# Optimization experiments

Measured on AMD Instinct MI355X. Metric: run time of the kernel, lower is better.

The kernel has to match this reference:

```python
import jax, jax.numpy as jnp
import numpy as np


def setup_inputs() -> dict:
    key = jax.random.key(0)
    k = jax.random.split(key, 5)
    B, S, D, H = 4, 2048, 2048, 8192
    scale1 = 1.0 / np.sqrt(D)
    scale2 = 1.0 / np.sqrt(H)
    return {
        "x": jax.random.normal(k[0], (B, S, D), dtype=jnp.float32),
        "w1": jax.random.normal(k[1], (H, D), dtype=jnp.float32) * scale1,
        "b1": jax.random.normal(k[2], (H,), dtype=jnp.float32) * scale1,
        "w2": jax.random.normal(k[3], (D, H), dtype=jnp.float32) * scale2,
        "b2": jax.random.normal(k[4], (D,), dtype=jnp.float32) * scale2,
    }


def reference(x, w1, b1, w2, b2):
    # fc1: [B,S,D] @ [D,H] -> [B,S,H]
    h = jnp.einsum("bsd,hd->bsh", x, w1) + b1
    # squared ReLU activation
    a = jnp.square(jax.nn.relu(h))
    # fc2: [B,S,H] @ [H,D] -> [B,S,D]
    return jnp.einsum("bsh,dh->bsd", a, w2) + b2
```

## Files before the change

### kernel.cpp

```cpp
#include <hip/hip_runtime.h>
#include <hip/hip_bf16.h>
#include <stdint.h>

typedef __bf16 bf16x8 __attribute__((ext_vector_type(8)));
typedef float f32x4 __attribute__((ext_vector_type(4)));


__device__ inline void gload_lds16(const void* g, void* lds) {
  __builtin_amdgcn_global_load_lds(
      (const __attribute__((address_space(1))) uint32_t*)(uintptr_t)g,
      (__attribute__((address_space(3))) uint32_t*)(uintptr_t)lds,
      16, 0, 0);
}

__device__ inline bf16x8 ds_readv(uint32_t addr) {
  bf16x8 r;
  asm volatile("ds_read_b128 %0, %1" : "=v"(r) : "v"(addr));
  return r;
}

#define LGKM(N) do {                                             \
    asm volatile("s_waitcnt lgkmcnt(" #N ")" ::: "memory");      \
    __builtin_amdgcn_sched_barrier(0);                           \
  } while (0)

__device__ inline short f2bf(float f) {
  union { float f; uint32_t u; } x; x.f = f;
  uint32_t u = x.u;
  u += 0x7fffu + ((u >> 16) & 1u);
  return (short)(u >> 16);
}

#define BAR() do { asm volatile("" ::: "memory"); \
                   __builtin_amdgcn_s_barrier();  \
                   asm volatile("" ::: "memory"); } while (0)


__global__ __launch_bounds__(256) void cvt_f32_bf16(
    const float* __restrict__ in, short* __restrict__ out, int n4) {
  int i = blockIdx.x * 256 + threadIdx.x;
  if (i < n4) {
    float4 v = reinterpret_cast<const float4*>(in)[i];
    short4 o;
    o.x = f2bf(v.x); o.y = f2bf(v.y); o.z = f2bf(v.z); o.w = f2bf(v.w);
    reinterpret_cast<short4*>(out)[i] = o;
  }
}


template <int EPI>
__global__ __launch_bounds__(512, 2) void gemm_bt(
    const short* __restrict__ A, const short* __restrict__ B,
    const float* __restrict__ bias, void* __restrict__ Cout,
    int M, int N, int K) {
  __shared__ __align__(16) short lds[2][4][128 * 64];

  const int tid  = threadIdx.x;
  const int wave = tid >> 6;
  const int lane = tid & 63;
  const int wr = wave >> 2;
  const int wc = wave & 3;
  const int fr = lane & 15, kq = lane >> 4;

  const int nwg = gridDim.x;
  const int w = (blockIdx.x & 7) * (nwg >> 3) + (blockIdx.x >> 3);
  const int gy = M >> 8;
  const int brow = w % gy;
  const int bcol = w / gy;

  f32x4 acc[8][4];
#pragma unroll
  for (int m = 0; m < 8; ++m)
#pragma unroll
    for (int n = 0; n < 4; ++n)
      acc[m][n] = (f32x4){0.f, 0.f, 0.f, 0.f};

  const int nk = K >> 6;

  const uint32_t LB = (uint32_t)(uintptr_t)&lds[0][0][0];
  uint32_t aA[4][2], aB[2][2];
#pragma unroll
  for (int m = 0; m < 4; ++m)
#pragma unroll
    for (int kk = 0; kk < 2; ++kk) {
      int r = wr * 64 + m * 16 + fr;
      int g = r * 8 + kk * 4 + kq;
      aA[m][kk] = LB + (uint32_t)((g ^ (r & 7)) * 16);
    }
#pragma unroll
  for (int n = 0; n < 2; ++n)
#pragma unroll
    for (int kk = 0; kk < 2; ++kk) {
      int r = wc * 32 + n * 16 + fr;
      int g = r * 8 + kk * 4 + kq;
      aB[n][kk] = LB + (uint32_t)((g ^ (r & 7)) * 16);
    }

  const int i0 = tid;
  const int gl0 = i0 ^ ((i0 >> 3) & 7);
  const int r0 = gl0 >> 3, c0 = gl0 & 7;
  const size_t rstep = (size_t)128 * K;

  const short* pA[2];
  const short* pB[2];
  {
    const int rb0 = (r0 >> 5) * 64 + (r0 & 31);
#pragma unroll
    for (int h = 0; h < 2; ++h) {
      pA[h] = A + (size_t)(brow * 256 + h * 64 + r0) * K + c0 * 8;
      pB[h] = B + (size_t)(bcol * 256 + rb0 + h * 32) * K + c0 * 8;
    }
  }

  const int dst0 = wave * 512, dst1 = 4096 + wave * 512;

#define STAGE(p, buf, slot)                              \
  do {                                                   \
    short* base_ = &lds[buf][slot][0];                   \
    gload_lds16((p), base_ + dst0);                      \
    gload_lds16((p) + rstep, base_ + dst1);              \
    (p) += 64;                                           \
  } while (0)

  STAGE(pA[0], 0, 0);
  STAGE(pA[1], 0, 1);
  STAGE(pB[0], 0, 2);
  STAGE(pB[1], 0, 3);
  asm volatile("s_waitcnt vmcnt(0)" ::: "memory");
  BAR();

  for (int t = 0; t < nk; ++t) {
    const int cur = t & 1, nxt = cur ^ 1;
    const bool s1 = (t + 1) < nk;

    if (s1) {
      STAGE(pA[0], nxt, 0);
      STAGE(pA[1], nxt, 1);
      STAGE(pB[0], nxt, 2);
      STAGE(pB[1], nxt, 3);
    }

    const uint32_t cb = (uint32_t)cur << 16;

    bf16x8 bq0[2][2], a0q[4][2], a1q[4][2], bq1[2][2];
#pragma unroll
    for (int n = 0; n < 2; ++n)
#pragma unroll
      for (int kk = 0; kk < 2; ++kk)
        bq0[n][kk] = ds_readv(aB[n][kk] + cb + 32768u);
#pragma unroll
    for (int m = 0; m < 4; ++m)
#pragma unroll
      for (int kk = 0; kk < 2; ++kk)
        a0q[m][kk] = ds_readv(aA[m][kk] + cb);
#pragma unroll
    for (int m = 0; m < 4; ++m)
#pragma unroll
      for (int kk = 0; kk < 2; ++kk)
        a1q[m][kk] = ds_readv(aA[m][kk] + cb + 16384u);
#pragma unroll
    for (int n = 0; n < 2; ++n)
#pragma unroll
      for (int kk = 0; kk < 2; ++kk)
        bq1[n][kk] = ds_readv(aB[n][kk] + cb + 49152u);

    LGKM(12);
    __builtin_amdgcn_s_setprio(1);
#pragma unroll
    for (int m = 0; m < 4; ++m)
#pragma unroll
      for (int n = 0; n < 2; ++n)
#pragma unroll
        for (int kk = 0; kk < 2; ++kk)
          acc[m][n] = __builtin_amdgcn_mfma_f32_16x16x32_bf16(
              bq0[n][kk], a0q[m][kk], acc[m][n], 0, 0, 0);
    __builtin_amdgcn_s_setprio(0);

    LGKM(4);
    __builtin_amdgcn_s_setprio(1);
#pragma unroll
    for (int m = 0; m < 4; ++m)
#pragma unroll
      for (int n = 0; n < 2; ++n)
#pragma unroll
        for (int kk = 0; kk < 2; ++kk)
          acc[m + 4][n] = __builtin_amdgcn_mfma_f32_16x16x32_bf16(
              bq0[n][kk], a1q[m][kk], acc[m + 4][n], 0, 0, 0);
    __builtin_amdgcn_s_setprio(0);

    LGKM(0);
    __builtin_amdgcn_s_setprio(1);
#pragma unroll
    for (int m = 0; m < 4; ++m)
#pragma unroll
      for (int n = 0; n < 2; ++n)
#pragma unroll
        for (int kk = 0; kk < 2; ++kk)
          acc[m + 4][n + 2] = __builtin_amdgcn_mfma_f32_16x16x32_bf16(
              bq1[n][kk], a1q[m][kk], acc[m + 4][n + 2], 0, 0, 0);
    __builtin_amdgcn_s_setprio(0);
    __builtin_amdgcn_s_setprio(1);
#pragma unroll
    for (int m = 0; m < 4; ++m)
#pragma unroll
      for (int n = 0; n < 2; ++n)
#pragma unroll
        for (int kk = 0; kk < 2; ++kk)
          acc[m][n + 2] = __builtin_amdgcn_mfma_f32_16x16x32_bf16(
              bq1[n][kk], a0q[m][kk], acc[m][n + 2], 0, 0, 0);
    __builtin_amdgcn_s_setprio(0);

    if (s1) {
      asm volatile("s_waitcnt vmcnt(0)" ::: "memory");
      BAR();
    }
  }

  const int q = lane >> 4;
  if (EPI == 0) {
    short* C = (short*)Cout;
#pragma unroll
    for (int m = 0; m < 8; ++m) {
      const int row = brow * 256 + wr * 128 + m * 16 + fr;
#pragma unroll
      for (int n = 0; n < 4; ++n) {
        const int col = bcol * 256 + wc * 64 + n * 16 + q * 4;
        const float4 bv = *(const float4*)&bias[col];
        short4 o;
        float v0 = acc[m][n][0] + bv.x; v0 = v0 > 0.f ? v0 * v0 : 0.f;
        float v1 = acc[m][n][1] + bv.y; v1 = v1 > 0.f ? v1 * v1 : 0.f;
        float v2 = acc[m][n][2] + bv.z; v2 = v2 > 0.f ? v2 * v2 : 0.f;
        float v3 = acc[m][n][3] + bv.w; v3 = v3 > 0.f ? v3 * v3 : 0.f;
        o.x = f2bf(v0); o.y = f2bf(v1); o.z = f2bf(v2); o.w = f2bf(v3);
        *(short4*)&C[(size_t)row * N + col] = o;
      }
    }
  } else {
    float* C = (float*)Cout;
#pragma unroll
    for (int m = 0; m < 8; ++m) {
      const int row = brow * 256 + wr * 128 + m * 16 + fr;
#pragma unroll
      for (int n = 0; n < 4; ++n) {
        const int col = bcol * 256 + wc * 64 + n * 16 + q * 4;
        const float4 bv = *(const float4*)&bias[col];
        float4 o;
        o.x = acc[m][n][0] + bv.x;
        o.y = acc[m][n][1] + bv.y;
        o.z = acc[m][n][2] + bv.z;
        o.w = acc[m][n][3] + bv.w;
        *(float4*)&C[(size_t)row * N + col] = o;
      }
    }
  }
#undef STAGE
}


extern "C" void kernel_launch(void* const* d_in, const int* in_sizes, int n_in,
                              void* d_out, int out_size, void* d_ws,
                              size_t ws_size, hipStream_t stream) {
  const float* x  = (const float*)d_in[0];
  const float* w1 = (const float*)d_in[1];
  const float* b1 = (const float*)d_in[2];
  const float* w2 = (const float*)d_in[3];
  const float* b2 = (const float*)d_in[4];
  float* out = (float*)d_out;

  const int H = in_sizes[2];
  const int D = in_sizes[4];
  const int M = in_sizes[0] / D;

  short* xb  = (short*)d_ws;
  short* w1b = xb  + (size_t)M * D;
  short* w2b = w1b + (size_t)H * D;
  short* act = w2b + (size_t)D * H;

  {
    int n4 = (M * D) / 4;
    cvt_f32_bf16<<<(n4 + 255) / 256, 256, 0, stream>>>(x, xb, n4);
    n4 = (H * D) / 4;
    cvt_f32_bf16<<<(n4 + 255) / 256, 256, 0, stream>>>(w1, w1b, n4);
    n4 = (D * H) / 4;
    cvt_f32_bf16<<<(n4 + 255) / 256, 256, 0, stream>>>(w2, w2b, n4);
  }

  gemm_bt<0><<<(M / 256) * (H / 256), 512, 0, stream>>>(
      xb, w1b, b1, (void*)act, M, H, D);
  gemm_bt<1><<<(M / 256) * (D / 256), 512, 0, stream>>>(
      act, w2b, b2, (void*)out, M, D, H);
}
```

Measured before the change: 572.7 us.

## Restructure GEMM main loop into 8-phase pipelined schedule with per-slot staging

Replaces the simple double-buffered K loop, which staged a whole tile and then waited on vmcnt(0) plus a barrier, with an unrolled two-tile schedule. Each tile is split into four MFMA quadrants, and each quadrant phase issues the global-to-LDS load for one sub-slot and waits with partial vmcnt counts. The aim is to overlap memory transfers with MFMA work at a finer grain and avoid full drains each iteration. In exchange there are many more barriers per tile, and correctness depends on the slot-reuse ordering and an even K tile count.

```diff
diff --git a/kernel.cpp b/kernel.cpp
--- a/kernel.cpp
+++ b/kernel.cpp
@@ -21,6 +21,10 @@
 
 #define LGKM(N) do {                                             \
     asm volatile("s_waitcnt lgkmcnt(" #N ")" ::: "memory");      \
+    __builtin_amdgcn_sched_barrier(0);                           \
+  } while (0)
+#define VM(N) do {                                               \
+    asm volatile("s_waitcnt vmcnt(" #N ")" ::: "memory");        \
     __builtin_amdgcn_sched_barrier(0);                           \
   } while (0)
 
@@ -122,50 +126,8 @@
     (p) += 64;                                           \
   } while (0)
 
-  STAGE(pA[0], 0, 0);
-  STAGE(pA[1], 0, 1);
-  STAGE(pB[0], 0, 2);
-  STAGE(pB[1], 0, 3);
-  asm volatile("s_waitcnt vmcnt(0)" ::: "memory");
-  BAR();
-
-  for (int t = 0; t < nk; ++t) {
-    const int cur = t & 1, nxt = cur ^ 1;
-    const bool s1 = (t + 1) < nk;
-
-    if (s1) {
-      STAGE(pA[0], nxt, 0);
-      STAGE(pA[1], nxt, 1);
-      STAGE(pB[0], nxt, 2);
-      STAGE(pB[1], nxt, 3);
-    }
-
-    const uint32_t cb = (uint32_t)cur << 16;
-
-    bf16x8 bq0[2][2], a0q[4][2], a1q[4][2], bq1[2][2];
-#pragma unroll
-    for (int n = 0; n < 2; ++n)
-#pragma unroll
-      for (int kk = 0; kk < 2; ++kk)
-        bq0[n][kk] = ds_readv(aB[n][kk] + cb + 32768u);
-#pragma unroll
-    for (int m = 0; m < 4; ++m)
-#pragma unroll
-      for (int kk = 0; kk < 2; ++kk)
-        a0q[m][kk] = ds_readv(aA[m][kk] + cb);
-#pragma unroll
-    for (int m = 0; m < 4; ++m)
-#pragma unroll
-      for (int kk = 0; kk < 2; ++kk)
-        a1q[m][kk] = ds_readv(aA[m][kk] + cb + 16384u);
-#pragma unroll
-    for (int n = 0; n < 2; ++n)
-#pragma unroll
-      for (int kk = 0; kk < 2; ++kk)
-        bq1[n][kk] = ds_readv(aB[n][kk] + cb + 49152u);
-
-    LGKM(12);
-    __builtin_amdgcn_s_setprio(1);
+  bf16x8 a0q[4][2], a1q[4][2], bq0[2][2], bq1[2][2];
+  auto Q1 = [&]() {
 #pragma unroll
     for (int m = 0; m < 4; ++m)
 #pragma unroll
@@ -174,10 +136,28 @@
         for (int kk = 0; kk < 2; ++kk)
           acc[m][n] = __builtin_amdgcn_mfma_f32_16x16x32_bf16(
               bq0[n][kk], a0q[m][kk], acc[m][n], 0, 0, 0);
-    __builtin_amdgcn_s_setprio(0);
-
-    LGKM(4);
-    __builtin_amdgcn_s_setprio(1);
+  };
+  auto Q2 = [&]() {
+#pragma unroll
+    for (int m = 0; m < 4; ++m)
+#pragma unroll
+      for (int n = 0; n < 2; ++n)
+#pragma unroll
+        for (int kk = 0; kk < 2; ++kk)
+          acc[m][n + 2] = __builtin_amdgcn_mfma_f32_16x16x32_bf16(
+              bq1[n][kk], a0q[m][kk], acc[m][n + 2], 0, 0, 0);
+  };
+  auto Q3 = [&]() {
+#pragma unroll
+    for (int m = 0; m < 4; ++m)
+#pragma unroll
+      for (int n = 0; n < 2; ++n)
+#pragma unroll
+        for (int kk = 0; kk < 2; ++kk)
+          acc[m + 4][n + 2] = __builtin_amdgcn_mfma_f32_16x16x32_bf16(
+              bq1[n][kk], a1q[m][kk], acc[m + 4][n + 2], 0, 0, 0);
+  };
+  auto Q4 = [&]() {
 #pragma unroll
     for (int m = 0; m < 4; ++m)
 #pragma unroll
@@ -186,35 +166,120 @@
         for (int kk = 0; kk < 2; ++kk)
           acc[m + 4][n] = __builtin_amdgcn_mfma_f32_16x16x32_bf16(
               bq0[n][kk], a1q[m][kk], acc[m + 4][n], 0, 0, 0);
-    __builtin_amdgcn_s_setprio(0);
-
-    LGKM(0);
-    __builtin_amdgcn_s_setprio(1);
-#pragma unroll
-    for (int m = 0; m < 4; ++m)
-#pragma unroll
-      for (int n = 0; n < 2; ++n)
-#pragma unroll
-        for (int kk = 0; kk < 2; ++kk)
-          acc[m + 4][n + 2] = __builtin_amdgcn_mfma_f32_16x16x32_bf16(
-              bq1[n][kk], a1q[m][kk], acc[m + 4][n + 2], 0, 0, 0);
-    __builtin_amdgcn_s_setprio(0);
-    __builtin_amdgcn_s_setprio(1);
-#pragma unroll
-    for (int m = 0; m < 4; ++m)
-#pragma unroll
-      for (int n = 0; n < 2; ++n)
-#pragma unroll
-        for (int kk = 0; kk < 2; ++kk)
-          acc[m][n + 2] = __builtin_amdgcn_mfma_f32_16x16x32_bf16(
-              bq1[n][kk], a0q[m][kk], acc[m][n + 2], 0, 0, 0);
-    __builtin_amdgcn_s_setprio(0);
-
-    if (s1) {
-      asm volatile("s_waitcnt vmcnt(0)" ::: "memory");
-      BAR();
-    }
-  }
+  };
+  auto RD_A0 = [&](uint32_t cb) {
+#pragma unroll
+    for (int m = 0; m < 4; ++m)
+#pragma unroll
+      for (int kk = 0; kk < 2; ++kk)
+        a0q[m][kk] = ds_readv(aA[m][kk] + cb);
+  };
+  auto RD_A1 = [&](uint32_t cb) {
+#pragma unroll
+    for (int m = 0; m < 4; ++m)
+#pragma unroll
+      for (int kk = 0; kk < 2; ++kk)
+        a1q[m][kk] = ds_readv(aA[m][kk] + cb + 16384u);
+  };
+  auto RD_B0 = [&](uint32_t cb) {
+#pragma unroll
+    for (int n = 0; n < 2; ++n)
+#pragma unroll
+      for (int kk = 0; kk < 2; ++kk)
+        bq0[n][kk] = ds_readv(aB[n][kk] + cb + 32768u);
+  };
+  auto RD_B1 = [&](uint32_t cb) {
+#pragma unroll
+    for (int n = 0; n < 2; ++n)
+#pragma unroll
+      for (int kk = 0; kk < 2; ++kk)
+        bq1[n][kk] = ds_readv(aB[n][kk] + cb + 49152u);
+  };
+
+#define PRIO_ON  __builtin_amdgcn_s_setprio(1)
+#define PRIO_OFF __builtin_amdgcn_s_setprio(0)
+
+  STAGE(pA[0], 0, 0);
+  STAGE(pB[0], 0, 2);
+  STAGE(pB[1], 0, 3);
+  STAGE(pA[1], 0, 1);
+  STAGE(pA[0], 1, 0);
+  STAGE(pB[0], 1, 2);
+  STAGE(pB[1], 1, 3);
+  VM(6);
+  BAR();
+
+  const int niter = nk >> 1;
+  for (int i = 0; i < niter - 1; ++i) {
+    RD_A0(0); RD_B0(0);
+    STAGE(pA[1], 1, 1);
+    LGKM(8);
+    BAR();
+    LGKM(0);
+    PRIO_ON; Q1(); PRIO_OFF;
+    VM(10); BAR();
+    RD_B1(0);
+    STAGE(pA[0], 0, 0);
+    BAR();
+    LGKM(0);
+    PRIO_ON; Q2(); PRIO_OFF;
+    VM(10); BAR();
+    RD_A1(0);
+    STAGE(pB[0], 0, 2);
+    BAR();
+    LGKM(0);
+    PRIO_ON; Q3(); PRIO_OFF;
+    VM(10); BAR();
+    STAGE(pB[1], 0, 3);
+    BAR();
+    PRIO_ON; Q4(); PRIO_OFF;
+    VM(10); BAR();
+
+    RD_A0(65536u); RD_B0(65536u);
+    STAGE(pA[1], 0, 1);
+    LGKM(8);
+    BAR();
+    LGKM(0);
+    PRIO_ON; Q1(); PRIO_OFF;
+    VM(10); BAR();
+    RD_B1(65536u);
+    STAGE(pA[0], 1, 0);
+    BAR();
+    LGKM(0);
+    PRIO_ON; Q2(); PRIO_OFF;
+    VM(10); BAR();
+    RD_A1(65536u);
+    STAGE(pB[0], 1, 2);
+    BAR();
+    LGKM(0);
+    PRIO_ON; Q3(); PRIO_OFF;
+    VM(10); BAR();
+    STAGE(pB[1], 1, 3);
+    BAR();
+    PRIO_ON; Q4(); PRIO_OFF;
+    VM(10); BAR();
+  }
+
+  RD_A0(0); RD_B0(0);
+  STAGE(pA[1], 1, 1);
+  LGKM(8);
+  BAR();
+  LGKM(0);
+  PRIO_ON; Q1(); PRIO_OFF;
+  VM(0); BAR();
+  RD_B1(0); BAR(); LGKM(0);
+  PRIO_ON; Q2(); PRIO_OFF; BAR();
+  RD_A1(0); BAR(); LGKM(0);
+  PRIO_ON; Q3(); PRIO_OFF; BAR();
+  PRIO_ON; Q4(); PRIO_OFF;
+  BAR();
+  RD_A0(65536u); RD_B0(65536u); BAR(); LGKM(0);
+  PRIO_ON; Q1(); PRIO_OFF; BAR();
+  RD_B1(65536u); BAR(); LGKM(0);
+  PRIO_ON; Q2(); PRIO_OFF; BAR();
+  RD_A1(65536u); BAR(); LGKM(0);
+  PRIO_ON; Q3(); PRIO_OFF; BAR();
+  PRIO_ON; Q4(); PRIO_OFF;
 
   const int q = lane >> 4;
   if (EPI == 0) {
```

Result: faster. 544.4 us (median of 3 runs) (-4.9%).

## Switch GEMM to 32x32x16 MFMA with quadrant-interleaved staged prefetch pipeline

Applied to the files above, without the earlier changes.

Replaces the 16x16x32 MFMA tiles with 32x32x16 tiles, so each wave holds 4x2 accumulator fragments of 16 floats and reads LDS with immediate offsets from precomputed swizzled bases. The main loop is split into four compute quadrants. Global-to-LDS loads for the next k-tiles are issued piecemeal between them, and the buffer slots are refilled as soon as each is consumed, with partial vmcnt waits instead of a full drain. This aims to overlap memory with MFMA work and cut LDS read traffic, at the cost of more barriers per iteration and more delicate slot-reuse correctness.

```diff
diff --git a/kernel.cpp b/kernel.cpp
--- a/kernel.cpp
+++ b/kernel.cpp
@@ -3,7 +3,7 @@
 #include <stdint.h>
 
 typedef __bf16 bf16x8 __attribute__((ext_vector_type(8)));
-typedef float f32x4 __attribute__((ext_vector_type(4)));
+typedef float f32x16 __attribute__((ext_vector_type(16)));
 
 
 __device__ inline void gload_lds16(const void* g, void* lds) {
@@ -13,14 +13,20 @@
       16, 0, 0);
 }
 
-__device__ inline bf16x8 ds_readv(uint32_t addr) {
-  bf16x8 r;
-  asm volatile("ds_read_b128 %0, %1" : "=v"(r) : "v"(addr));
-  return r;
-}
+#define DSR(dst, base, OFF)                                         \
+  asm volatile("ds_read_b128 %0, %1 offset:" #OFF                   \
+               : "=v"(dst) : "v"(base))
+#define RD4(arr, base, OFF) do {                                    \
+    DSR(arr[0], base[0], OFF); DSR(arr[1], base[1], OFF);           \
+    DSR(arr[2], base[2], OFF); DSR(arr[3], base[3], OFF);           \
+  } while (0)
 
 #define LGKM(N) do {                                             \
     asm volatile("s_waitcnt lgkmcnt(" #N ")" ::: "memory");      \
+    __builtin_amdgcn_sched_barrier(0);                           \
+  } while (0)
+#define VM(N) do {                                               \
+    asm volatile("s_waitcnt vmcnt(" #N ")" ::: "memory");        \
     __builtin_amdgcn_sched_barrier(0);                           \
   } while (0)
 
@@ -60,7 +66,7 @@
   const int lane = tid & 63;
   const int wr = wave >> 2;
   const int wc = wave & 3;
-  const int fr = lane & 15, kq = lane >> 4;
+  const int l31 = lane & 31, kh = lane >> 5;
 
   const int nwg = gridDim.x;
   const int w = (blockIdx.x & 7) * (nwg >> 3) + (blockIdx.x >> 3);
@@ -68,33 +74,31 @@
   const int brow = w % gy;
   const int bcol = w / gy;
 
-  f32x4 acc[8][4];
-#pragma unroll
-  for (int m = 0; m < 8; ++m)
-#pragma unroll
-    for (int n = 0; n < 4; ++n)
-      acc[m][n] = (f32x4){0.f, 0.f, 0.f, 0.f};
+  f32x16 acc[4][2];
+#pragma unroll
+  for (int m = 0; m < 4; ++m)
+#pragma unroll
+    for (int n = 0; n < 2; ++n) {
+      f32x16 z = {0.f};
+      acc[m][n] = z;
+    }
 
   const int nk = K >> 6;
 
   const uint32_t LB = (uint32_t)(uintptr_t)&lds[0][0][0];
-  uint32_t aA[4][2], aB[2][2];
-#pragma unroll
-  for (int m = 0; m < 4; ++m)
-#pragma unroll
-    for (int kk = 0; kk < 2; ++kk) {
-      int r = wr * 64 + m * 16 + fr;
-      int g = r * 8 + kk * 4 + kq;
-      aA[m][kk] = LB + (uint32_t)((g ^ (r & 7)) * 16);
-    }
-#pragma unroll
-  for (int n = 0; n < 2; ++n)
-#pragma unroll
-    for (int kk = 0; kk < 2; ++kk) {
-      int r = wc * 32 + n * 16 + fr;
-      int g = r * 8 + kk * 4 + kq;
-      aB[n][kk] = LB + (uint32_t)((g ^ (r & 7)) * 16);
-    }
+  uint32_t aT[4], bT[4];
+  {
+    const int r  = wr * 64 + l31;
+    const int x  = r & 7;
+    const int rb = wc * 32 + l31;
+    const int xb = rb & 7;
+#pragma unroll
+    for (int ks = 0; ks < 4; ++ks) {
+      aT[ks] = LB + (uint32_t)(r * 128 + (((ks * 2 + kh) ^ x) * 16));
+      bT[ks] = LB + 32768u +
+               (uint32_t)(rb * 128 + (((ks * 2 + kh) ^ xb) * 16));
+    }
+  }
 
   const int i0 = tid;
   const int gl0 = i0 ^ ((i0 >> 3) & 7);
@@ -122,134 +126,137 @@
     (p) += 64;                                           \
   } while (0)
 
+  bf16x8 a01[2][4], a23[2][4], b0[4], b1[4];
+  auto Q1 = [&]() {
+#pragma unroll
+    for (int mi = 0; mi < 2; ++mi)
+#pragma unroll
+      for (int ks = 0; ks < 4; ++ks)
+        acc[mi][0] = __builtin_amdgcn_mfma_f32_32x32x16_bf16(
+            b0[ks], a01[mi][ks], acc[mi][0], 0, 0, 0);
+  };
+  auto Q2 = [&]() {
+#pragma unroll
+    for (int mi = 0; mi < 2; ++mi)
+#pragma unroll
+      for (int ks = 0; ks < 4; ++ks)
+        acc[mi][1] = __builtin_amdgcn_mfma_f32_32x32x16_bf16(
+            b1[ks], a01[mi][ks], acc[mi][1], 0, 0, 0);
+  };
+  auto Q3 = [&]() {
+#pragma unroll
+    for (int mi = 0; mi < 2; ++mi)
+#pragma unroll
+      for (int ks = 0; ks < 4; ++ks)
+        acc[2 + mi][1] = __builtin_amdgcn_mfma_f32_32x32x16_bf16(
+            b1[ks], a23[mi][ks], acc[2 + mi][1], 0, 0, 0);
+  };
+  auto Q4 = [&]() {
+#pragma unroll
+    for (int mi = 0; mi < 2; ++mi)
+#pragma unroll
+      for (int ks = 0; ks < 4; ++ks)
+        acc[2 + mi][0] = __builtin_amdgcn_mfma_f32_32x32x16_bf16(
+            b0[ks], a23[mi][ks], acc[2 + mi][0], 0, 0, 0);
+  };
+
+#define PRIO_ON  __builtin_amdgcn_s_setprio(1)
+#define PRIO_OFF __builtin_amdgcn_s_setprio(0)
+
   STAGE(pA[0], 0, 0);
-  STAGE(pA[1], 0, 1);
   STAGE(pB[0], 0, 2);
   STAGE(pB[1], 0, 3);
-  asm volatile("s_waitcnt vmcnt(0)" ::: "memory");
+  STAGE(pA[1], 0, 1);
+  STAGE(pA[0], 1, 0);
+  STAGE(pB[0], 1, 2);
+  STAGE(pB[1], 1, 3);
+  VM(6);
   BAR();
 
   for (int t = 0; t < nk; ++t) {
     const int cur = t & 1, nxt = cur ^ 1;
-    const bool s1 = (t + 1) < nk;
-
-    if (s1) {
-      STAGE(pA[0], nxt, 0);
-      STAGE(pA[1], nxt, 1);
-      STAGE(pB[0], nxt, 2);
-      STAGE(pB[1], nxt, 3);
-    }
-
-    const uint32_t cb = (uint32_t)cur << 16;
-
-    bf16x8 bq0[2][2], a0q[4][2], a1q[4][2], bq1[2][2];
-#pragma unroll
-    for (int n = 0; n < 2; ++n)
-#pragma unroll
-      for (int kk = 0; kk < 2; ++kk)
-        bq0[n][kk] = ds_readv(aB[n][kk] + cb + 32768u);
-#pragma unroll
-    for (int m = 0; m < 4; ++m)
-#pragma unroll
-      for (int kk = 0; kk < 2; ++kk)
-        a0q[m][kk] = ds_readv(aA[m][kk] + cb);
-#pragma unroll
-    for (int m = 0; m < 4; ++m)
-#pragma unroll
-      for (int kk = 0; kk < 2; ++kk)
-        a1q[m][kk] = ds_readv(aA[m][kk] + cb + 16384u);
-#pragma unroll
-    for (int n = 0; n < 2; ++n)
-#pragma unroll
-      for (int kk = 0; kk < 2; ++kk)
-        bq1[n][kk] = ds_readv(aB[n][kk] + cb + 49152u);
-
-    LGKM(12);
-    __builtin_amdgcn_s_setprio(1);
-#pragma unroll
-    for (int m = 0; m < 4; ++m)
-#pragma unroll
-      for (int n = 0; n < 2; ++n)
-#pragma unroll
-        for (int kk = 0; kk < 2; ++kk)
-          acc[m][n] = __builtin_amdgcn_mfma_f32_16x16x32_bf16(
-              bq0[n][kk], a0q[m][kk], acc[m][n], 0, 0, 0);
-    __builtin_amdgcn_s_setprio(0);
-
-    LGKM(4);
-    __builtin_amdgcn_s_setprio(1);
-#pragma unroll
-    for (int m = 0; m < 4; ++m)
-#pragma unroll
-      for (int n = 0; n < 2; ++n)
-#pragma unroll
-        for (int kk = 0; kk < 2; ++kk)
-          acc[m + 4][n] = __builtin_amdgcn_mfma_f32_16x16x32_bf16(
-              bq0[n][kk], a1q[m][kk], acc[m + 4][n], 0, 0, 0);
-    __builtin_amdgcn_s_setprio(0);
-
+    const bool s1 = (t + 1) < nk, g2 = (t + 2) < nk;
+    if (t) {
+      const int32_t d = cur ? 65536 : -65536;
+#pragma unroll
+      for (int ks = 0; ks < 4; ++ks) { aT[ks] += d; bT[ks] += d; }
+    }
+
+    RD4(a01[0], aT, 0);
+    RD4(a01[1], aT, 4096);
+    RD4(b0, bT, 0);
+    if (s1) STAGE(pA[1], nxt, 1);
+    LGKM(8);
+    BAR();
     LGKM(0);
-    __builtin_amdgcn_s_setprio(1);
-#pragma unroll
-    for (int m = 0; m < 4; ++m)
-#pragma unroll
-      for (int n = 0; n < 2; ++n)
-#pragma unroll
-        for (int kk = 0; kk < 2; ++kk)
-          acc[m + 4][n + 2] = __builtin_amdgcn_mfma_f32_16x16x32_bf16(
-              bq1[n][kk], a1q[m][kk], acc[m + 4][n + 2], 0, 0, 0);
-    __builtin_amdgcn_s_setprio(0);
-    __builtin_amdgcn_s_setprio(1);
-#pragma unroll
-    for (int m = 0; m < 4; ++m)
-#pragma unroll
-      for (int n = 0; n < 2; ++n)
-#pragma unroll
-        for (int kk = 0; kk < 2; ++kk)
-          acc[m][n + 2] = __builtin_amdgcn_mfma_f32_16x16x32_bf16(
-              bq1[n][kk], a0q[m][kk], acc[m][n + 2], 0, 0, 0);
-    __builtin_amdgcn_s_setprio(0);
-
-    if (s1) {
-      asm volatile("s_waitcnt vmcnt(0)" ::: "memory");
-      BAR();
-    }
-  }
-
-  const int q = lane >> 4;
+    PRIO_ON; Q1(); PRIO_OFF;
+    BAR();
+
+    RD4(b1, bT, 16384);
+    if (g2) STAGE(pA[0], cur, 0);
+    BAR();
+    LGKM(0);
+    PRIO_ON; Q2(); PRIO_OFF;
+    BAR();
+
+    RD4(a23[0], aT, 16384);
+    RD4(a23[1], aT, 20480);
+    if (g2) STAGE(pB[0], cur, 2);
+    BAR();
+    LGKM(0);
+    PRIO_ON; Q3(); PRIO_OFF;
+    BAR();
+
+    if (g2) STAGE(pB[1], cur, 3);
+    BAR();
+    PRIO_ON; Q4(); PRIO_OFF;
+    if (g2)      { VM(6); }
+    else if (s1) { VM(0); }
+    if (s1) BAR();
+  }
+
+  const int hi = lane >> 5;
   if (EPI == 0) {
     short* C = (short*)Cout;
 #pragma unroll
-    for (int m = 0; m < 8; ++m) {
-      const int row = brow * 256 + wr * 128 + m * 16 + fr;
-#pragma unroll
-      for (int n = 0; n < 4; ++n) {
-        const int col = bcol * 256 + wc * 64 + n * 16 + q * 4;
-        const float4 bv = *(const float4*)&bias[col];
-        short4 o;
-        float v0 = acc[m][n][0] + bv.x; v0 = v0 > 0.f ? v0 * v0 : 0.f;
-        float v1 = acc[m][n][1] + bv.y; v1 = v1 > 0.f ? v1 * v1 : 0.f;
-        float v2 = acc[m][n][2] + bv.z; v2 = v2 > 0.f ? v2 * v2 : 0.f;
-        float v3 = acc[m][n][3] + bv.w; v3 = v3 > 0.f ? v3 * v3 : 0.f;
-        o.x = f2bf(v0); o.y = f2bf(v1); o.z = f2bf(v2); o.w = f2bf(v3);
-        *(short4*)&C[(size_t)row * N + col] = o;
+    for (int mf = 0; mf < 4; ++mf) {
+      const int row = brow * 256 + wr * 128 + mf * 32 + l31;
+#pragma unroll
+      for (int nf = 0; nf < 2; ++nf) {
+        const int colb = bcol * 256 + wc * 64 + nf * 32 + hi * 4;
+#pragma unroll
+        for (int g = 0; g < 4; ++g) {
+          const int col = colb + g * 8;
+          const float4 bv = *(const float4*)&bias[col];
+          short4 o;
+          float v0 = acc[mf][nf][4 * g + 0] + bv.x; v0 = v0 > 0.f ? v0 * v0 : 0.f;
+          float v1 = acc[mf][nf][4 * g + 1] + bv.y; v1 = v1 > 0.f ? v1 * v1 : 0.f;
+          float v2 = acc[mf][nf][4 * g + 2] + bv.z; v2 = v2 > 0.f ? v2 * v2 : 0.f;
+          float v3 = acc[mf][nf][4 * g + 3] + bv.w; v3 = v3 > 0.f ? v3 * v3 : 0.f;
+          o.x = f2bf(v0); o.y = f2bf(v1); o.z = f2bf(v2); o.w = f2bf(v3);
+          *(short4*)&C[(size_t)row * N + col] = o;
+        }
       }
     }
   } else {
     float* C = (float*)Cout;
 #pragma unroll
-    for (int m = 0; m < 8; ++m) {
-      const int row = brow * 256 + wr * 128 + m * 16 + fr;
-#pragma unroll
-      for (int n = 0; n < 4; ++n) {
-        const int col = bcol * 256 + wc * 64 + n * 16 + q * 4;
-        const float4 bv = *(const float4*)&bias[col];
-        float4 o;
-        o.x = acc[m][n][0] + bv.x;
-        o.y = acc[m][n][1] + bv.y;
-        o.z = acc[m][n][2] + bv.z;
-        o.w = acc[m][n][3] + bv.w;
-        *(float4*)&C[(size_t)row * N + col] = o;
+    for (int mf = 0; mf < 4; ++mf) {
+      const int row = brow * 256 + wr * 128 + mf * 32 + l31;
+#pragma unroll
+      for (int nf = 0; nf < 2; ++nf) {
+        const int colb = bcol * 256 + wc * 64 + nf * 32 + hi * 4;
+#pragma unroll
+        for (int g = 0; g < 4; ++g) {
+          const int col = colb + g * 8;
+          const float4 bv = *(const float4*)&bias[col];
+          float4 o;
+          o.x = acc[mf][nf][4 * g + 0] + bv.x;
+          o.y = acc[mf][nf][4 * g + 1] + bv.y;
+          o.z = acc[mf][nf][4 * g + 2] + bv.z;
+          o.w = acc[mf][nf][4 * g + 3] + bv.w;
+          *(float4*)&C[(size_t)row * N + col] = o;
+        }
       }
     }
   }
```

Result: slower. 650.5 us (+13.6%).

## Interleave per-quadrant LDS reads, global prefetch and MFMA with finer barriers

Applied to the files above, without the earlier changes.

The main loop is reorganised into four compute quadrants. Each quadrant loads its own LDS fragments and issues one slot of the next tile's global-to-LDS prefetch, so slots are refilled as soon as they are consumed. The prologue now prefetches most of two k-tiles ahead, and vmcnt waits are partial rather than full drains. LDS addresses use base registers plus immediate offsets instead of per-fragment address arrays, which cuts VGPR use. The cost is many more workgroup barriers per iteration and tricky slot-reuse ordering, which could cause stalls or races if any dependency is mis-sequenced.

```diff
diff --git a/kernel.cpp b/kernel.cpp
--- a/kernel.cpp
+++ b/kernel.cpp
@@ -13,14 +13,16 @@
       16, 0, 0);
 }
 
-__device__ inline bf16x8 ds_readv(uint32_t addr) {
-  bf16x8 r;
-  asm volatile("ds_read_b128 %0, %1" : "=v"(r) : "v"(addr));
-  return r;
-}
+#define DSR(dst, base, OFF)                                         \
+  asm volatile("ds_read_b128 %0, %1 offset:" #OFF                   \
+               : "=v"(dst) : "v"(base))
 
 #define LGKM(N) do {                                             \
     asm volatile("s_waitcnt lgkmcnt(" #N ")" ::: "memory");      \
+    __builtin_amdgcn_sched_barrier(0);                           \
+  } while (0)
+#define VM(N) do {                                               \
+    asm volatile("s_waitcnt vmcnt(" #N ")" ::: "memory");        \
     __builtin_amdgcn_sched_barrier(0);                           \
   } while (0)
 
@@ -78,23 +80,15 @@
   const int nk = K >> 6;
 
   const uint32_t LB = (uint32_t)(uintptr_t)&lds[0][0][0];
-  uint32_t aA[4][2], aB[2][2];
-#pragma unroll
-  for (int m = 0; m < 4; ++m)
-#pragma unroll
-    for (int kk = 0; kk < 2; ++kk) {
-      int r = wr * 64 + m * 16 + fr;
-      int g = r * 8 + kk * 4 + kq;
-      aA[m][kk] = LB + (uint32_t)((g ^ (r & 7)) * 16);
-    }
-#pragma unroll
-  for (int n = 0; n < 2; ++n)
-#pragma unroll
-    for (int kk = 0; kk < 2; ++kk) {
-      int r = wc * 32 + n * 16 + fr;
-      int g = r * 8 + kk * 4 + kq;
-      aB[n][kk] = LB + (uint32_t)((g ^ (r & 7)) * 16);
-    }
+  uint32_t bA[2], bB[2];
+  {
+    const uint32_t x0 = (uint32_t)(((kq)     ^ (fr & 7)) * 16);
+    const uint32_t x1 = (uint32_t)(((4 + kq) ^ (fr & 7)) * 16);
+    const uint32_t ra = (uint32_t)((wr * 64 + fr) * 128);
+    const uint32_t rb = (uint32_t)((wc * 32 + fr) * 128);
+    bA[0] = LB + ra + x0;            bA[1] = LB + ra + x1;
+    bB[0] = LB + 32768u + rb + x0;   bB[1] = LB + 32768u + rb + x1;
+  }
 
   const int i0 = tid;
   const int gl0 = i0 ^ ((i0 >> 3) & 7);
@@ -122,98 +116,106 @@
     (p) += 64;                                           \
   } while (0)
 
+  bf16x8 a0q[4][2], a1q[4][2], bq0[2][2], bq1[2][2];
+  auto Q1 = [&]() {
+#pragma unroll
+    for (int m = 0; m < 4; ++m)
+#pragma unroll
+      for (int n = 0; n < 2; ++n)
+#pragma unroll
+        for (int kk = 0; kk < 2; ++kk)
+          acc[m][n] = __builtin_amdgcn_mfma_f32_16x16x32_bf16(
+              bq0[n][kk], a0q[m][kk], acc[m][n], 0, 0, 0);
+  };
+  auto Q2 = [&]() {
+#pragma unroll
+    for (int m = 0; m < 4; ++m)
+#pragma unroll
+      for (int n = 0; n < 2; ++n)
+#pragma unroll
+        for (int kk = 0; kk < 2; ++kk)
+          acc[m][n + 2] = __builtin_amdgcn_mfma_f32_16x16x32_bf16(
+              bq1[n][kk], a0q[m][kk], acc[m][n + 2], 0, 0, 0);
+  };
+  auto Q3 = [&]() {
+#pragma unroll
+    for (int m = 0; m < 4; ++m)
+#pragma unroll
+      for (int n = 0; n < 2; ++n)
+#pragma unroll
+        for (int kk = 0; kk < 2; ++kk)
+          acc[m + 4][n + 2] = __builtin_amdgcn_mfma_f32_16x16x32_bf16(
+              bq1[n][kk], a1q[m][kk], acc[m + 4][n + 2], 0, 0, 0);
+  };
+  auto Q4 = [&]() {
+#pragma unroll
+    for (int m = 0; m < 4; ++m)
+#pragma unroll
+      for (int n = 0; n < 2; ++n)
+#pragma unroll
+        for (int kk = 0; kk < 2; ++kk)
+          acc[m + 4][n] = __builtin_amdgcn_mfma_f32_16x16x32_bf16(
+              bq0[n][kk], a1q[m][kk], acc[m + 4][n], 0, 0, 0);
+  };
+
+#define PRIO_ON  __builtin_amdgcn_s_setprio(1)
+#define PRIO_OFF __builtin_amdgcn_s_setprio(0)
+
   STAGE(pA[0], 0, 0);
-  STAGE(pA[1], 0, 1);
   STAGE(pB[0], 0, 2);
   STAGE(pB[1], 0, 3);
-  asm volatile("s_waitcnt vmcnt(0)" ::: "memory");
+  STAGE(pA[1], 0, 1);
+  STAGE(pA[0], 1, 0);
+  STAGE(pB[0], 1, 2);
+  STAGE(pB[1], 1, 3);
+  VM(6);
   BAR();
 
   for (int t = 0; t < nk; ++t) {
     const int cur = t & 1, nxt = cur ^ 1;
-    const bool s1 = (t + 1) < nk;
-
-    if (s1) {
-      STAGE(pA[0], nxt, 0);
-      STAGE(pA[1], nxt, 1);
-      STAGE(pB[0], nxt, 2);
-      STAGE(pB[1], nxt, 3);
-    }
-
-    const uint32_t cb = (uint32_t)cur << 16;
-
-    bf16x8 bq0[2][2], a0q[4][2], a1q[4][2], bq1[2][2];
-#pragma unroll
-    for (int n = 0; n < 2; ++n)
-#pragma unroll
-      for (int kk = 0; kk < 2; ++kk)
-        bq0[n][kk] = ds_readv(aB[n][kk] + cb + 32768u);
-#pragma unroll
-    for (int m = 0; m < 4; ++m)
-#pragma unroll
-      for (int kk = 0; kk < 2; ++kk)
-        a0q[m][kk] = ds_readv(aA[m][kk] + cb);
-#pragma unroll
-    for (int m = 0; m < 4; ++m)
-#pragma unroll
-      for (int kk = 0; kk < 2; ++kk)
-        a1q[m][kk] = ds_readv(aA[m][kk] + cb + 16384u);
-#pragma unroll
-    for (int n = 0; n < 2; ++n)
-#pragma unroll
-      for (int kk = 0; kk < 2; ++kk)
-        bq1[n][kk] = ds_readv(aB[n][kk] + cb + 49152u);
-
-    LGKM(12);
-    __builtin_amdgcn_s_setprio(1);
-#pragma unroll
-    for (int m = 0; m < 4; ++m)
-#pragma unroll
-      for (int n = 0; n < 2; ++n)
-#pragma unroll
-        for (int kk = 0; kk < 2; ++kk)
-          acc[m][n] = __builtin_amdgcn_mfma_f32_16x16x32_bf16(
-              bq0[n][kk], a0q[m][kk], acc[m][n], 0, 0, 0);
-    __builtin_amdgcn_s_setprio(0);
-
-    LGKM(4);
-    __builtin_amdgcn_s_setprio(1);
-#pragma unroll
-    for (int m = 0; m < 4; ++m)
-#pragma unroll
-      for (int n = 0; n < 2; ++n)
-#pragma unroll
-        for (int kk = 0; kk < 2; ++kk)
-          acc[m + 4][n] = __builtin_amdgcn_mfma_f32_16x16x32_bf16(
-              bq0[n][kk], a1q[m][kk], acc[m + 4][n], 0, 0, 0);
-    __builtin_amdgcn_s_setprio(0);
-
+    const bool s1 = (t + 1) < nk, g2 = (t + 2) < nk;
+    if (t) {
+      const int32_t d = cur ? 65536 : -65536;
+      bA[0] += d; bA[1] += d; bB[0] += d; bB[1] += d;
+    }
+
+    DSR(a0q[0][0], bA[0], 0);     DSR(a0q[0][1], bA[1], 0);
+    DSR(a0q[1][0], bA[0], 2048);  DSR(a0q[1][1], bA[1], 2048);
+    DSR(a0q[2][0], bA[0], 4096);  DSR(a0q[2][1], bA[1], 4096);
+    DSR(a0q[3][0], bA[0], 6144);  DSR(a0q[3][1], bA[1], 6144);
+    DSR(bq0[0][0], bB[0], 0);     DSR(bq0[0][1], bB[1], 0);
+    DSR(bq0[1][0], bB[0], 2048);  DSR(bq0[1][1], bB[1], 2048);
+    if (s1) STAGE(pA[1], nxt, 1);
+    LGKM(8);
+    BAR();
     LGKM(0);
-    __builtin_amdgcn_s_setprio(1);
-#pragma unroll
-    for (int m = 0; m < 4; ++m)
-#pragma unroll
-      for (int n = 0; n < 2; ++n)
-#pragma unroll
-        for (int kk = 0; kk < 2; ++kk)
-          acc[m + 4][n + 2] = __builtin_amdgcn_mfma_f32_16x16x32_bf16(
-              bq1[n][kk], a1q[m][kk], acc[m + 4][n + 2], 0, 0, 0);
-    __builtin_amdgcn_s_setprio(0);
-    __builtin_amdgcn_s_setprio(1);
-#pragma unroll
-    for (int m = 0; m < 4; ++m)
-#pragma unroll
-      for (int n = 0; n < 2; ++n)
-#pragma unroll
-        for (int kk = 0; kk < 2; ++kk)
-          acc[m][n + 2] = __builtin_amdgcn_mfma_f32_16x16x32_bf16(
-              bq1[n][kk], a0q[m][kk], acc[m][n + 2], 0, 0, 0);
-    __builtin_amdgcn_s_setprio(0);
-
-    if (s1) {
-      asm volatile("s_waitcnt vmcnt(0)" ::: "memory");
-      BAR();
-    }
+    PRIO_ON; Q1(); PRIO_OFF;
+    BAR();
+
+    DSR(bq1[0][0], bB[0], 16384); DSR(bq1[0][1], bB[1], 16384);
+    DSR(bq1[1][0], bB[0], 18432); DSR(bq1[1][1], bB[1], 18432);
+    if (g2) STAGE(pA[0], cur, 0);
+    BAR();
+    LGKM(0);
+    PRIO_ON; Q2(); PRIO_OFF;
+    BAR();
+
+    DSR(a1q[0][0], bA[0], 16384); DSR(a1q[0][1], bA[1], 16384);
+    DSR(a1q[1][0], bA[0], 18432); DSR(a1q[1][1], bA[1], 18432);
+    DSR(a1q[2][0], bA[0], 20480); DSR(a1q[2][1], bA[1], 20480);
+    DSR(a1q[3][0], bA[0], 22528); DSR(a1q[3][1], bA[1], 22528);
+    if (g2) STAGE(pB[0], cur, 2);
+    BAR();
+    LGKM(0);
+    PRIO_ON; Q3(); PRIO_OFF;
+    BAR();
+
+    if (g2) STAGE(pB[1], cur, 3);
+    BAR();
+    PRIO_ON; Q4(); PRIO_OFF;
+    if (g2)      { VM(6); }
+    else if (s1) { VM(0); }
+    if (s1) BAR();
   }
 
   const int q = lane >> 4;
```

After: 547.9 us. -4.3%, faster.
